# Optimization experiments

Measured on AMD Instinct MI355X. Metric: run time of the kernel, lower is better.

Reference implementation:

```python
import jax, jax.numpy as jnp
import numpy as np

N_NODES = 50000
N_EDGES = 1250000
D_IN = 256
D_OUT = 64


def setup_inputs() -> dict:
    key = jax.random.key(0)
    k0, k1, k2, k3, k4 = jax.random.split(key, 5)
    return {
        "arg0_1": jax.random.normal(k0, (D_OUT, D_IN), dtype=jnp.float32),
        "arg1_1": jax.random.normal(k1, (D_OUT,), dtype=jnp.float32),
        "arg2_1": jax.random.randint(k2, (2, N_EDGES), 0, N_NODES, dtype=jnp.int64),
        "arg3_1": jax.random.uniform(k3, (N_EDGES,), dtype=jnp.float32),
        "arg4_1": jax.random.normal(k4, (N_NODES, D_IN), dtype=jnp.float32),
    }


def reference(arg0_1, arg1_1, arg2_1, arg3_1, arg4_1):
    # h = x @ W^T  : [N, D_OUT]
    h = jnp.matmul(arg4_1, arg0_1.T)
    src = arg2_1[0]  # gather indices
    dst = arg2_1[1]  # scatter_add indices
    # edge messages: gather source rows, scale by edge weight  : [E, D_OUT]
    msg = arg3_1[:, None] * h[src]
    # scatter_add into node buckets
    agg = jax.ops.segment_sum(msg, dst, num_segments=N_NODES)
    return agg + arg1_1
```

## Files before the change

### kernel.cpp

```cpp
#include <hip/hip_runtime.h>
#include <hip/hip_bf16.h>

#define D_IN    256
#define D_OUT   64
#define NNODES  50000
#define NEDGES  1250000

#define BUCK_SHIFT 8
#define BUCK_NODES 256
#define NBUCK      196
#define CPAD       16
#define EPB        4096
#define NB_EDGE    ((NEDGES + EPB - 1) / EPB)
#define GEMM_BLOCKS ((NNODES + 63) / 64)
#define BCAP    8128

typedef float f32x4 __attribute__((ext_vector_type(4)));
typedef short s16x8 __attribute__((ext_vector_type(8)));

static __device__ __forceinline__ unsigned short f2bf(float f) {
    union { float f; unsigned u; } v; v.f = f;
    unsigned r = v.u + 0x7FFFu + ((v.u >> 16) & 1u);
    return (unsigned short)(r >> 16);
}

__global__ __launch_bounds__(256) void gemm_bin(
    const float* __restrict__ x, const float* __restrict__ W,
    signed char* __restrict__ hq, float* __restrict__ scale_tab, int N,
    const int* __restrict__ src, const int* __restrict__ dst,
    const float* __restrict__ wt,
    int* __restrict__ bcursor, unsigned long long* __restrict__ binned)
{
    __shared__ uint4 sW[2048];
    __shared__ int   lcnt[NBUCK];
    __shared__ int   lbase[NBUCK];

    const int t = threadIdx.x;

    if (blockIdx.x >= GEMM_BLOCKS) {
        for (int i = t; i < NBUCK; i += 256) lcnt[i] = 0;
        __syncthreads();

        int base = (blockIdx.x - GEMM_BLOCKS) * EPB;
        bool full = (base + EPB <= NEDGES);

        if (full) {
            const int4* d4 = (const int4*)(dst + base);
            #pragma unroll
            for (int it = 0; it < 4; ++it) {
                int4 d = d4[t + it * 256];
                atomicAdd(&lcnt[d.x >> BUCK_SHIFT], 1);
                atomicAdd(&lcnt[d.y >> BUCK_SHIFT], 1);
                atomicAdd(&lcnt[d.z >> BUCK_SHIFT], 1);
                atomicAdd(&lcnt[d.w >> BUCK_SHIFT], 1);
            }
        } else {
            for (int e = base + t; e < NEDGES; e += 256)
                atomicAdd(&lcnt[dst[e] >> BUCK_SHIFT], 1);
        }
        __syncthreads();

        if (t < NBUCK) {
            int c = lcnt[t];
            lbase[t] = c ? (t * BCAP + atomicAdd(&bcursor[t * CPAD], c)) : 0;
            lcnt[t]  = 0;
        }
        __syncthreads();

        if (full) {
            const int4*   s4 = (const int4*)(src + base);
            const int4*   d4 = (const int4*)(dst + base);
            const float4* w4 = (const float4*)(wt + base);
            #pragma unroll
            for (int it = 0; it < 4; ++it) {
                int4   ss = s4[t + it * 256];
                int4   dd = d4[t + it * 256];
                float4 ww = w4[t + it * 256];
                int sv[4]   = {ss.x, ss.y, ss.z, ss.w};
                int dv[4]   = {dd.x, dd.y, dd.z, dd.w};
                float wv[4] = {ww.x, ww.y, ww.z, ww.w};
                #pragma unroll
                for (int k = 0; k < 4; ++k) {
                    int d = dv[k];
                    int b = d >> BUCK_SHIFT;
                    int r = atomicAdd(&lcnt[b], 1);
                    unsigned lo = (unsigned)sv[k] | ((unsigned)(d & (BUCK_NODES - 1)) << 16);
                    unsigned long long rec = (unsigned long long)lo
                                           | ((unsigned long long)__float_as_uint(wv[k]) << 32);
                    binned[lbase[b] + r] = rec;
                }
            }
        } else {
            for (int e = base + t; e < NEDGES; e += 256) {
                int d = dst[e];
                int b = d >> BUCK_SHIFT;
                int r = atomicAdd(&lcnt[b], 1);
                int sidx = src[e];
                unsigned lo = (unsigned)sidx | ((unsigned)(d & (BUCK_NODES - 1)) << 16);
                unsigned long long rec = (unsigned long long)lo
                                       | ((unsigned long long)__float_as_uint(wt[e]) << 32);
                binned[lbase[b] + r] = rec;
            }
        }
        return;
    }

    const int lane = t & 63;
    const int wave = t >> 6;
    const int m    = lane & 15;
    const int q    = lane >> 4;

    #pragma unroll
    for (int i = 0; i < 8; ++i) {
        int slot = t + i * 256;
        int ln   = slot & 63;
        int kb   = (slot >> 6) & 7;
        int c    = slot >> 9;
        int lm = ln & 15, lq = ln >> 4;
        const float* wp = W + (c * 16 + lm) * D_IN + kb * 32 + lq * 8;
        float4 w0 = *(const float4*)wp;
        float4 w1 = *(const float4*)(wp + 4);
        uint4 u;
        u.x = (unsigned)f2bf(w0.x) | ((unsigned)f2bf(w0.y) << 16);
        u.y = (unsigned)f2bf(w0.z) | ((unsigned)f2bf(w0.w) << 16);
        u.z = (unsigned)f2bf(w1.x) | ((unsigned)f2bf(w1.y) << 16);
        u.w = (unsigned)f2bf(w1.z) | ((unsigned)f2bf(w1.w) << 16);
        sW[slot] = u;
    }
    __syncthreads();

    const int rowA = blockIdx.x * 64 + wave * 16 + m;
    const int rowc = (rowA < N) ? rowA : (N - 1);
    const float* xr = x + (long long)rowc * D_IN + q * 8;

    f32x4 acc[4] = {};

    #pragma unroll
    for (int kb = 0; kb < 8; ++kb) {
        float4 a0 = *(const float4*)(xr + kb * 32);
        float4 a1 = *(const float4*)(xr + kb * 32 + 4);
        s16x8 af;
        af[0] = (short)f2bf(a0.x); af[1] = (short)f2bf(a0.y);
        af[2] = (short)f2bf(a0.z); af[3] = (short)f2bf(a0.w);
        af[4] = (short)f2bf(a1.x); af[5] = (short)f2bf(a1.y);
        af[6] = (short)f2bf(a1.z); af[7] = (short)f2bf(a1.w);

        #pragma unroll
        for (int c = 0; c < 4; ++c) {
            s16x8 bf = *(const s16x8*)&sW[(c * 8 + kb) * 64 + lane];
            acc[c] = __builtin_amdgcn_mfma_f32_16x16x32_bf16(af, bf, acc[c], 0, 0, 0);
        }
    }

    #pragma unroll
    for (int r = 0; r < 4; ++r) {
        float local = fmaxf(fmaxf(fabsf(acc[0][r]), fabsf(acc[1][r])),
                            fmaxf(fabsf(acc[2][r]), fabsf(acc[3][r])));
        #pragma unroll
        for (int msk = 1; msk < 16; msk <<= 1)
            local = fmaxf(local, __shfl_xor(local, msk));
        float amax = fmaxf(local, 1e-6f);
        float inv  = 127.0f / amax;
        int gr = blockIdx.x * 64 + wave * 16 + q * 4 + r;
        if (gr < N) {
            if (m == 0) scale_tab[gr] = amax * (1.0f / 127.0f);
            #pragma unroll
            for (int c = 0; c < 4; ++c) {
                int qv = __float2int_rn(acc[c][r] * inv);
                hq[(long long)gr * D_OUT + c * 16 + m] = (signed char)qv;
            }
        }
    }
}

__global__ __launch_bounds__(512) void sort_buckets(
    const unsigned long long* __restrict__ binned, const int* __restrict__ bcursor,
    const float* __restrict__ scale_tab,
    unsigned long long* __restrict__ csr,
    int* __restrict__ starts, int* __restrict__ counts)
{
    __shared__ int s[256];
    __shared__ int lcnt[BUCK_NODES];
    __shared__ int lcur[BUCK_NODES];
    __shared__ int sh_s0, sh_cnt;
    int t = threadIdx.x;
    int b = blockIdx.x;

    int v = 0;
    if (t < 256) {
        v = (t < NBUCK) ? bcursor[t * CPAD] : 0;
        s[t] = v;
        lcnt[t] = 0;
    }
    __syncthreads();
    #pragma unroll
    for (int off = 1; off < 256; off <<= 1) {
        int u = (t < 256 && t >= off) ? s[t - off] : 0;
        __syncthreads();
        if (t < 256) s[t] += u;
        __syncthreads();
    }
    if (t == b) { sh_s0 = s[t] - v; sh_cnt = v; }
    __syncthreads();
    int s0 = sh_s0, cntb = sh_cnt;
    int node0 = b << BUCK_SHIFT;
    int nn = min(BUCK_NODES, NNODES - node0);
    const unsigned long long* bsrc = binned + (long long)b * BCAP;

    for (int k = t; k < cntb; k += 512)
        atomicAdd(&lcnt[(int)((bsrc[k] >> 16) & 0xFF)], 1);
    __syncthreads();

    int v2 = 0;
    if (t < 256) { v2 = lcnt[t]; s[t] = v2; }
    __syncthreads();
    #pragma unroll
    for (int off = 1; off < 256; off <<= 1) {
        int u = (t < 256 && t >= off) ? s[t - off] : 0;
        __syncthreads();
        if (t < 256) s[t] += u;
        __syncthreads();
    }
    if (t < 256) {
        int excl = s[t] - v2;
        lcur[t] = s0 + excl;
        if (t < nn) {
            starts[node0 + t] = s0 + excl;
            counts[node0 + t] = v2;
        }
    }
    __syncthreads();

    for (int k = t; k < cntb; k += 512) {
        unsigned long long r = bsrc[k];
        int dloc = (int)((r >> 16) & 0xFF);
        int sidx = (int)(r & 0xFFFF);
        float wf = __uint_as_float((unsigned)(r >> 32)) * scale_tab[sidx];
        int pos  = atomicAdd(&lcur[dloc], 1);
        csr[pos] = (r & 0xFFFFFFFFull)
                 | ((unsigned long long)__float_as_uint(wf) << 32);
    }
}

__global__ __launch_bounds__(256) void agg_nodes(
    const int2* __restrict__ recs, const int* __restrict__ starts,
    const int* __restrict__ counts, const signed char* __restrict__ hq,
    const float* __restrict__ bias, float* __restrict__ out)
{
    int wid  = (blockIdx.x * 256 + threadIdx.x) >> 6;
    int node = __builtin_amdgcn_readfirstlane(wid);
    if (node >= NNODES) return;
    int lane = threadIdx.x & 63;

    float acc = bias[lane];
    int s0  = starts[node];
    int cnt = counts[node];
    int i = s0, e = s0 + cnt;

    for (; i + 7 < e; i += 8) {
        int2 r0 = recs[i + 0];
        int2 r1 = recs[i + 1];
        int2 r2 = recs[i + 2];
        int2 r3 = recs[i + 3];
        int2 r4 = recs[i + 4];
        int2 r5 = recs[i + 5];
        int2 r6 = recs[i + 6];
        int2 r7 = recs[i + 7];
        float v0 = (float)hq[(r0.x & 0xFFFF) * D_OUT + lane];
        float v1 = (float)hq[(r1.x & 0xFFFF) * D_OUT + lane];
        float v2 = (float)hq[(r2.x & 0xFFFF) * D_OUT + lane];
        float v3 = (float)hq[(r3.x & 0xFFFF) * D_OUT + lane];
        float v4 = (float)hq[(r4.x & 0xFFFF) * D_OUT + lane];
        float v5 = (float)hq[(r5.x & 0xFFFF) * D_OUT + lane];
        float v6 = (float)hq[(r6.x & 0xFFFF) * D_OUT + lane];
        float v7 = (float)hq[(r7.x & 0xFFFF) * D_OUT + lane];
        acc += __int_as_float(r0.y) * v0;
        acc += __int_as_float(r1.y) * v1;
        acc += __int_as_float(r2.y) * v2;
        acc += __int_as_float(r3.y) * v3;
        acc += __int_as_float(r4.y) * v4;
        acc += __int_as_float(r5.y) * v5;
        acc += __int_as_float(r6.y) * v6;
        acc += __int_as_float(r7.y) * v7;
    }
    for (; i + 3 < e; i += 4) {
        int2 r0 = recs[i + 0];
        int2 r1 = recs[i + 1];
        int2 r2 = recs[i + 2];
        int2 r3 = recs[i + 3];
        float v0 = (float)hq[(r0.x & 0xFFFF) * D_OUT + lane];
        float v1 = (float)hq[(r1.x & 0xFFFF) * D_OUT + lane];
        float v2 = (float)hq[(r2.x & 0xFFFF) * D_OUT + lane];
        float v3 = (float)hq[(r3.x & 0xFFFF) * D_OUT + lane];
        acc += __int_as_float(r0.y) * v0;
        acc += __int_as_float(r1.y) * v1;
        acc += __int_as_float(r2.y) * v2;
        acc += __int_as_float(r3.y) * v3;
    }
    for (; i < e; ++i) {
        int2 r = recs[i];
        acc += __int_as_float(r.y) * (float)hq[(r.x & 0xFFFF) * D_OUT + lane];
    }
    out[(long long)node * D_OUT + lane] = acc;
}

__global__ __launch_bounds__(256) void init_bias(
    float* __restrict__ out, const float* __restrict__ bias, int total)
{
    int i = blockIdx.x * blockDim.x + threadIdx.x;
    if (i < total) out[i] = bias[i & (D_OUT - 1)];
}

__global__ __launch_bounds__(256) void scatter_edges(
    const int* __restrict__ src, const int* __restrict__ dst,
    const float* __restrict__ wt, const signed char* __restrict__ hq,
    const float* __restrict__ scale_tab, float* __restrict__ out)
{
    long long gid = (long long)blockIdx.x * blockDim.x + threadIdx.x;
    int e    = (int)(gid >> 6);
    int lane = threadIdx.x & 63;
    if (e < NEDGES) {
        int   s = src[e];
        int   d = dst[e];
        float w = wt[e] * scale_tab[s];
        float v = w * (float)hq[(long long)s * D_OUT + lane];
        atomicAdd(&out[(long long)d * D_OUT + lane], v);
    }
}

extern "C" void kernel_launch(void* const* d_in, const int* in_sizes, int n_in,
                              void* d_out, int out_size, void* d_ws, size_t ws_size,
                              hipStream_t stream)
{
    const float* W     = (const float*)d_in[0];
    const float* bias  = (const float*)d_in[1];
    const int*   edges = (const int*)  d_in[2];
    const float* wt    = (const float*)d_in[3];
    const float* x     = (const float*)d_in[4];
    float*       out   = (float*)d_out;

    const int* src = edges;
    const int* dst = edges + NEDGES;

    char* ws = (char*)d_ws;
    const size_t OFF_HQ     = 0;
    const size_t OFF_SCALE  = 3200000;
    const size_t OFF_RECS   = 3400000;
    const size_t OFF_STARTS = 13400000;
    const size_t OFF_COUNTS = 13600000;
    const size_t OFF_BCUR   = 13800000;
    const size_t REQUIRED   = 13812544;

    signed char* hq        = (signed char*)(ws + OFF_HQ);
    float*       scale_tab = (float*)(ws + OFF_SCALE);

    if (ws_size >= REQUIRED) {
        unsigned long long* csr     = (unsigned long long*)(ws + OFF_RECS);
        int*                starts  = (int*)(ws + OFF_STARTS);
        int*                counts  = (int*)(ws + OFF_COUNTS);
        int*                bcursor = (int*)(ws + OFF_BCUR);

        unsigned long long* binned = (unsigned long long*)d_out;

        hipMemsetAsync(bcursor, 0, NBUCK * CPAD * sizeof(int), stream);

        gemm_bin<<<GEMM_BLOCKS + NB_EDGE, 256, 0, stream>>>(
            x, W, hq, scale_tab, NNODES, src, dst, wt, bcursor, binned);

        sort_buckets<<<NBUCK, 512, 0, stream>>>(binned, bcursor, scale_tab,
                                                csr, starts, counts);

        int nb = (NNODES * 64 + 255) / 256;
        agg_nodes<<<nb, 256, 0, stream>>>((const int2*)csr, starts, counts,
                                          hq, bias, out);
    } else {
        gemm_bin<<<GEMM_BLOCKS, 256, 0, stream>>>(
            x, W, hq, scale_tab, NNODES,
            (const int*)nullptr, (const int*)nullptr, (const float*)nullptr,
            (int*)nullptr, (unsigned long long*)nullptr);
        int total = NNODES * D_OUT;
        init_bias<<<(total + 255) / 256, 256, 0, stream>>>(out, bias, total);
        long long threads = (long long)NEDGES * 64;
        int blocks = (int)((threads + 255) / 256);
        scatter_edges<<<blocks, 256, 0, stream>>>(src, dst, wt, hq, scale_tab, out);
    }
}
```

Before: 170.0 us.

## Shrink edge-binning blocks, schedule them first, and share LDS with GEMM

Edges per binning block drop from 4096 to 1024, so there are four times as many smaller binning blocks, and they now come before the GEMM blocks in the fused launch. The GEMM weight tile and the binning counters now share one LDS union, which lowers per-block shared memory. The aim is to start the latency-bound binning work earlier and spread it across more CUs so it overlaps with the GEMM. The cost is more global atomics on the bucket cursors (four times as many blocks reserve ranges) and more fragmented writes into each bucket.

```diff
diff --git a/kernel.cpp b/kernel.cpp
--- a/kernel.cpp
+++ b/kernel.cpp
@@ -10,7 +10,7 @@
 #define BUCK_NODES 256
 #define NBUCK      196
 #define CPAD       16
-#define EPB        4096
+#define EPB        1024
 #define NB_EDGE    ((NEDGES + EPB - 1) / EPB)
 #define GEMM_BLOCKS ((NNODES + 63) / 64)
 #define BCAP    8128
@@ -29,82 +29,75 @@
     signed char* __restrict__ hq, float* __restrict__ scale_tab, int N,
     const int* __restrict__ src, const int* __restrict__ dst,
     const float* __restrict__ wt,
-    int* __restrict__ bcursor, unsigned long long* __restrict__ binned)
-{
-    __shared__ uint4 sW[2048];
-    __shared__ int   lcnt[NBUCK];
-    __shared__ int   lbase[NBUCK];
+    int* __restrict__ bcursor, unsigned long long* __restrict__ binned,
+    int nbin)
+{
+    __shared__ union {
+        uint4 sW[2048];
+        struct { int lcnt[NBUCK]; int lbase[NBUCK]; } bin;
+    } sh;
 
     const int t = threadIdx.x;
 
-    if (blockIdx.x >= GEMM_BLOCKS) {
-        for (int i = t; i < NBUCK; i += 256) lcnt[i] = 0;
-        __syncthreads();
-
-        int base = (blockIdx.x - GEMM_BLOCKS) * EPB;
+    if ((int)blockIdx.x < nbin) {
+        if (t < NBUCK) { sh.bin.lcnt[t] = 0; }
+        __syncthreads();
+
+        int base = blockIdx.x * EPB;
         bool full = (base + EPB <= NEDGES);
 
         if (full) {
-            const int4* d4 = (const int4*)(dst + base);
-            #pragma unroll
-            for (int it = 0; it < 4; ++it) {
-                int4 d = d4[t + it * 256];
-                atomicAdd(&lcnt[d.x >> BUCK_SHIFT], 1);
-                atomicAdd(&lcnt[d.y >> BUCK_SHIFT], 1);
-                atomicAdd(&lcnt[d.z >> BUCK_SHIFT], 1);
-                atomicAdd(&lcnt[d.w >> BUCK_SHIFT], 1);
-            }
+            int4 d = ((const int4*)(dst + base))[t];
+            atomicAdd(&sh.bin.lcnt[d.x >> BUCK_SHIFT], 1);
+            atomicAdd(&sh.bin.lcnt[d.y >> BUCK_SHIFT], 1);
+            atomicAdd(&sh.bin.lcnt[d.z >> BUCK_SHIFT], 1);
+            atomicAdd(&sh.bin.lcnt[d.w >> BUCK_SHIFT], 1);
         } else {
             for (int e = base + t; e < NEDGES; e += 256)
-                atomicAdd(&lcnt[dst[e] >> BUCK_SHIFT], 1);
+                atomicAdd(&sh.bin.lcnt[dst[e] >> BUCK_SHIFT], 1);
         }
         __syncthreads();
 
         if (t < NBUCK) {
-            int c = lcnt[t];
-            lbase[t] = c ? (t * BCAP + atomicAdd(&bcursor[t * CPAD], c)) : 0;
-            lcnt[t]  = 0;
+            int c = sh.bin.lcnt[t];
+            sh.bin.lbase[t] = c ? (t * BCAP + atomicAdd(&bcursor[t * CPAD], c)) : 0;
+            sh.bin.lcnt[t]  = 0;
         }
         __syncthreads();
 
         if (full) {
-            const int4*   s4 = (const int4*)(src + base);
-            const int4*   d4 = (const int4*)(dst + base);
-            const float4* w4 = (const float4*)(wt + base);
+            int4   ss = ((const int4*)(src + base))[t];
+            int4   dd = ((const int4*)(dst + base))[t];
+            float4 ww = ((const float4*)(wt + base))[t];
+            int sv[4]   = {ss.x, ss.y, ss.z, ss.w};
+            int dv[4]   = {dd.x, dd.y, dd.z, dd.w};
+            float wv[4] = {ww.x, ww.y, ww.z, ww.w};
             #pragma unroll
-            for (int it = 0; it < 4; ++it) {
-                int4   ss = s4[t + it * 256];
-                int4   dd = d4[t + it * 256];
-                float4 ww = w4[t + it * 256];
-                int sv[4]   = {ss.x, ss.y, ss.z, ss.w};
-                int dv[4]   = {dd.x, dd.y, dd.z, dd.w};
-                float wv[4] = {ww.x, ww.y, ww.z, ww.w};
-                #pragma unroll
-                for (int k = 0; k < 4; ++k) {
-                    int d = dv[k];
-                    int b = d >> BUCK_SHIFT;
-                    int r = atomicAdd(&lcnt[b], 1);
-                    unsigned lo = (unsigned)sv[k] | ((unsigned)(d & (BUCK_NODES - 1)) << 16);
-                    unsigned long long rec = (unsigned long long)lo
-                                           | ((unsigned long long)__float_as_uint(wv[k]) << 32);
-                    binned[lbase[b] + r] = rec;
-                }
+            for (int k = 0; k < 4; ++k) {
+                int d = dv[k];
+                int b = d >> BUCK_SHIFT;
+                int r = atomicAdd(&sh.bin.lcnt[b], 1);
+                unsigned lo = (unsigned)sv[k] | ((unsigned)(d & (BUCK_NODES - 1)) << 16);
+                unsigned long long rec = (unsigned long long)lo
+                                       | ((unsigned long long)__float_as_uint(wv[k]) << 32);
+                binned[sh.bin.lbase[b] + r] = rec;
             }
         } else {
             for (int e = base + t; e < NEDGES; e += 256) {
                 int d = dst[e];
                 int b = d >> BUCK_SHIFT;
-                int r = atomicAdd(&lcnt[b], 1);
+                int r = atomicAdd(&sh.bin.lcnt[b], 1);
                 int sidx = src[e];
                 unsigned lo = (unsigned)sidx | ((unsigned)(d & (BUCK_NODES - 1)) << 16);
                 unsigned long long rec = (unsigned long long)lo
                                        | ((unsigned long long)__float_as_uint(wt[e]) << 32);
-                binned[lbase[b] + r] = rec;
+                binned[sh.bin.lbase[b] + r] = rec;
             }
         }
         return;
     }
 
+    const int gb   = (int)blockIdx.x - nbin;
     const int lane = t & 63;
     const int wave = t >> 6;
     const int m    = lane & 15;
@@ -125,11 +118,11 @@
         u.y = (unsigned)f2bf(w0.z) | ((unsigned)f2bf(w0.w) << 16);
         u.z = (unsigned)f2bf(w1.x) | ((unsigned)f2bf(w1.y) << 16);
         u.w = (unsigned)f2bf(w1.z) | ((unsigned)f2bf(w1.w) << 16);
-        sW[slot] = u;
-    }
-    __syncthreads();
-
-    const int rowA = blockIdx.x * 64 + wave * 16 + m;
+        sh.sW[slot] = u;
+    }
+    __syncthreads();
+
+    const int rowA = gb * 64 + wave * 16 + m;
     const int rowc = (rowA < N) ? rowA : (N - 1);
     const float* xr = x + (long long)rowc * D_IN + q * 8;
 
@@ -147,7 +140,7 @@
 
         #pragma unroll
         for (int c = 0; c < 4; ++c) {
-            s16x8 bf = *(const s16x8*)&sW[(c * 8 + kb) * 64 + lane];
+            s16x8 bf = *(const s16x8*)&sh.sW[(c * 8 + kb) * 64 + lane];
             acc[c] = __builtin_amdgcn_mfma_f32_16x16x32_bf16(af, bf, acc[c], 0, 0, 0);
         }
     }
@@ -161,7 +154,7 @@
             local = fmaxf(local, __shfl_xor(local, msk));
         float amax = fmaxf(local, 1e-6f);
         float inv  = 127.0f / amax;
-        int gr = blockIdx.x * 64 + wave * 16 + q * 4 + r;
+        int gr = gb * 64 + wave * 16 + q * 4 + r;
         if (gr < N) {
             if (m == 0) scale_tab[gr] = amax * (1.0f / 127.0f);
             #pragma unroll
@@ -364,8 +357,9 @@
 
         hipMemsetAsync(bcursor, 0, NBUCK * CPAD * sizeof(int), stream);
 
-        gemm_bin<<<GEMM_BLOCKS + NB_EDGE, 256, 0, stream>>>(
-            x, W, hq, scale_tab, NNODES, src, dst, wt, bcursor, binned);
+        gemm_bin<<<NB_EDGE + GEMM_BLOCKS, 256, 0, stream>>>(
+            x, W, hq, scale_tab, NNODES, src, dst, wt, bcursor, binned,
+            NB_EDGE);
 
         sort_buckets<<<NBUCK, 512, 0, stream>>>(binned, bcursor, scale_tab,
                                                 csr, starts, counts);
@@ -377,7 +371,7 @@
         gemm_bin<<<GEMM_BLOCKS, 256, 0, stream>>>(
             x, W, hq, scale_tab, NNODES,
             (const int*)nullptr, (const int*)nullptr, (const float*)nullptr,
-            (int*)nullptr, (unsigned long long*)nullptr);
+            (int*)nullptr, (unsigned long long*)nullptr, 0);
         int total = NNODES * D_OUT;
         init_bias<<<(total + 255) / 256, 256, 0, stream>>>(out, bias, total);
         long long threads = (long long)NEDGES * 64;
```

New measurement: 183.9 us. 8.1% more time.
